# Kernel optimization log

Hardware: AMD Instinct MI355X
Metric: run time of the kernel (lower is better)

The kernel has to match this reference:

```python
import jax, jax.numpy as jnp
import numpy as np

B, P, ENC = 128, 196, 2048
D, A, ED, V, L = 512, 512, 512, 10000, 20


def setup_inputs() -> dict:
    key = jax.random.key(0)
    ks = jax.random.split(key, 24)
    s = 0.02
    inp = {
        'encoder_out': jax.random.normal(ks[0], (B, P, ENC), jnp.float32),
        'captions': jax.random.randint(ks[1], (B, L), 0, V),
        'caption_len': jax.random.randint(ks[2], (B,), 2, L + 1).at[0].set(L),
        # embedding (uniform(-0.1, 0.1) per init_weights)
        'emb_w': jax.random.uniform(ks[3], (V, ED), jnp.float32, -0.1, 0.1),
        # LSTMCell: input = ED + ENC, hidden = D, gates order i,f,g,o
        'Wih': jax.random.normal(ks[4], (4 * D, ED + ENC), jnp.float32) * s,
        'Whh': jax.random.normal(ks[5], (4 * D, D), jnp.float32) * s,
        'bih': jax.random.normal(ks[6], (4 * D,), jnp.float32) * s,
        'bhh': jax.random.normal(ks[7], (4 * D,), jnp.float32) * s,
        # init hidden state projections
        'h0_w': jax.random.normal(ks[8], (D, ENC), jnp.float32) * s,
        'h0_b': jnp.zeros((D,), jnp.float32),
        'c0_w': jax.random.normal(ks[9], (D, ENC), jnp.float32) * s,
        'c0_b': jnp.zeros((D,), jnp.float32),
        # gate D -> ENC
        'gate_w': jax.random.normal(ks[10], (ENC, D), jnp.float32) * s,
        'gate_b': jnp.zeros((ENC,), jnp.float32),
        # output projection D -> V (uniform(-0.1,0.1), bias 0 per init_weights)
        'lin_w': jax.random.uniform(ks[11], (V, D), jnp.float32, -0.1, 0.1),
        'lin_b': jnp.zeros((V,), jnp.float32),
        # attention network
        'ea_w': jax.random.normal(ks[12], (A, ENC), jnp.float32) * s,
        'ea_b': jnp.zeros((A,), jnp.float32),
        'da_w': jax.random.normal(ks[13], (A, D), jnp.float32) * s,
        'da_b': jnp.zeros((A,), jnp.float32),
        'fa_w': jax.random.normal(ks[14], (1, A), jnp.float32) * s,
        'fa_b': jnp.zeros((1,), jnp.float32),
    }
    return inp


def reference(encoder_out, captions, caption_len, emb_w, Wih, Whh, bih, bhh,
              h0_w, h0_b, c0_w, c0_b, gate_w, gate_b, lin_w, lin_b,
              ea_w, ea_b, da_w, da_b, fa_w, fa_b):
    # sort by caption length descending (as in torch .sort(descending=True))
    order = jnp.argsort(-caption_len)
    cap_len = caption_len[order]
    enc = encoder_out[order]            # [B, P, ENC]
    caps = captions[order]              # [B, L]
    dec_len = cap_len - 1               # per-example decode lengths

    emb = emb_w[caps]                   # [B, L, ED]
    mean_enc = enc.mean(axis=1)         # [B, ENC]
    h0 = mean_enc @ h0_w.T + h0_b       # [B, D]
    c0 = mean_enc @ c0_w.T + c0_b
    att1 = enc @ ea_w.T + ea_b          # [B, P, A] precomputed encoder attention

    T = caps.shape[1] - 1               # static max decode steps (caption_len[0]=L)

    def step(carry, i):
        h, c = carry
        # Bahdanau attention
        att2 = h @ da_w.T + da_b                                   # [B, A]
        e = (jax.nn.relu(att1 + att2[:, None, :]) @ fa_w.T + fa_b)[..., 0]  # [B, P]
        alpha = jax.nn.softmax(e, axis=1)
        awe = jnp.einsum('bp,bpe->be', alpha, enc)                 # [B, ENC]
        g = jax.nn.sigmoid(h @ gate_w.T + gate_b)
        awe = g * awe
        # LSTMCell
        x = jnp.concatenate([emb[:, i, :], awe], axis=1)           # [B, ED+ENC]
        gates = x @ Wih.T + bih + h @ Whh.T + bhh                  # [B, 4D]
        gi, gf, gg, go = jnp.split(gates, 4, axis=1)
        c_new = jax.nn.sigmoid(gf) * c + jax.nn.sigmoid(gi) * jnp.tanh(gg)
        h_new = jax.nn.sigmoid(go) * jnp.tanh(c_new)
        active = (i < dec_len)[:, None]                            # ragged mask
        # inactive rows keep old state (matches h[:batch_size_i] slicing)
        h2 = jnp.where(active, h_new, h)
        c2 = jnp.where(active, c_new, c)
        # dropout is identity in eval; output projection masked to zeros
        pred = jnp.where(active, h_new @ lin_w.T + lin_b, 0.0)     # [B, V]
        alpha = jnp.where(active, alpha, 0.0)
        return (h2, c2), (pred, alpha)

    (_, _), (preds, alphas) = jax.lax.scan(step, (h0, c0), jnp.arange(T))
    pred = jnp.swapaxes(preds, 0, 1)     # [B, T, V]
    alphas = jnp.swapaxes(alphas, 0, 1)  # [B, T, P]
    return pred, caps, dec_len, alphas, order
```

## Files before the change

kernel.cpp:

```cpp
#include <hip/hip_runtime.h>
#include <hip/hip_bf16.h>
#include <math.h>

#define Bn 128
#define Pn 196
#define ENCn 2048
#define Dn 512
#define An 512
#define EDn 512
#define Vn 10000
#define Ln 20
#define Tn 19

typedef short v8s __attribute__((ext_vector_type(8)));
typedef float v4f __attribute__((ext_vector_type(4)));

__device__ __forceinline__ float sigf(float x){ return 1.f/(1.f+__expf(-x)); }
__device__ __forceinline__ unsigned short f2bf(float f){
  unsigned u = __float_as_uint(f);
  return (unsigned short)((u + 0x7FFFu + ((u>>16)&1u)) >> 16);
}
__device__ __forceinline__ float bf2f(unsigned short h){
  return __uint_as_float(((unsigned)h)<<16);
}


__global__ void k_order(const int* __restrict__ caption_len,
                        const int* __restrict__ captions,
                        int* __restrict__ order_i, int* __restrict__ declen_i,
                        int* __restrict__ caps_s,
                        float* __restrict__ out_caps, float* __restrict__ out_declen,
                        float* __restrict__ out_order)
{
  __shared__ int lens[Bn];
  int b = threadIdx.x;
  lens[b] = caption_len[b];
  __syncthreads();
  int lb = lens[b];
  int r = 0;
  for (int j = 0; j < Bn; ++j) {
    int lj = lens[j];
    r += (int)((lj > lb) || (lj == lb && j < b));
  }
  order_i[r] = b;
  declen_i[r] = lb - 1;
  out_order[r] = (float)b;
  out_declen[r] = (float)(lb - 1);
  for (int t = 0; t < Ln; ++t) {
    int cv = captions[b*Ln + t];
    caps_s[r*Ln + t] = cv;
    out_caps[r*Ln + t] = (float)cv;
  }
}

__global__ void k_setup_bias(const float* __restrict__ bih, const float* __restrict__ bhh,
                             const float* __restrict__ da_b, const float* __restrict__ gate_b,
                             const float* __restrict__ h0_b, const float* __restrict__ c0_b,
                             float* __restrict__ bsum_r, float* __restrict__ dg_b,
                             float* __restrict__ hc_b)
{
  int i = blockIdx.x*256 + threadIdx.x;
  if (i < 2048) {
    int d = i >> 2, g = i & 3;
    bsum_r[i] = bih[g*512+d] + bhh[g*512+d];
  }
  if (i < 2560) dg_b[i] = (i < 512) ? da_b[i] : gate_b[i-512];
  if (i < 1024) hc_b[i] = (i < 512) ? h0_b[i] : c0_b[i-512];
}

__global__ void k_cvt(const float* __restrict__ src, unsigned short* __restrict__ dst, int n)
{
  int i = (blockIdx.x*256 + threadIdx.x)*4;
  if (i < n) {
    float4 v = *(const float4*)(src + i);
    dst[i+0]=f2bf(v.x); dst[i+1]=f2bf(v.y); dst[i+2]=f2bf(v.z); dst[i+3]=f2bf(v.w);
  }
}

__global__ void k_wcat(const float* __restrict__ Wih, const float* __restrict__ Whh,
                       unsigned short* __restrict__ dst)
{
  int i = (blockIdx.x*256 + threadIdx.x)*4;
  if (i >= 2048*3072) return;
  int rp = i/3072, j = i - rp*3072;
  int d = rp >> 2, g = rp & 3;
  int r = g*512 + d;
  const float* s = (j < 2560) ? (Wih + (size_t)r*2560 + j) : (Whh + (size_t)r*512 + (j-2560));
  float4 v = *(const float4*)s;
  dst[i+0]=f2bf(v.x); dst[i+1]=f2bf(v.y); dst[i+2]=f2bf(v.z); dst[i+3]=f2bf(v.w);
}

__global__ void k_cvt_enc(const float* __restrict__ enc, const int* __restrict__ order_i,
                          unsigned short* __restrict__ dst)
{
  int id = blockIdx.x;
  int b = id / Pn, p = id - b*Pn;
  const float* src = enc + ((size_t)order_i[b]*Pn + p)*ENCn;
  unsigned short* d = dst + (size_t)id*ENCn;
  int i = threadIdx.x*8;
  float4 v0 = *(const float4*)(src+i), v1 = *(const float4*)(src+i+4);
  d[i+0]=f2bf(v0.x); d[i+1]=f2bf(v0.y); d[i+2]=f2bf(v0.z); d[i+3]=f2bf(v0.w);
  d[i+4]=f2bf(v1.x); d[i+5]=f2bf(v1.y); d[i+6]=f2bf(v1.z); d[i+7]=f2bf(v1.w);
}

__global__ void k_mean(const unsigned short* __restrict__ enc_bf,
                       unsigned short* __restrict__ mean_bf)
{
  int b = blockIdx.x;
  const unsigned short* eb = enc_bf + (size_t)b*Pn*ENCn;
  for (int e = threadIdx.x; e < ENCn; e += 256) {
    float s = 0.f;
    for (int p = 0; p < Pn; ++p) s += bf2f(eb[(size_t)p*ENCn + e]);
    mean_bf[b*ENCn + e] = f2bf(s * (1.f/196.f));
  }
}

__global__ void k_zero(uint4* __restrict__ p, int n)
{
  int i = blockIdx.x*256 + threadIdx.x;
  if (i < n) p[i] = uint4{0,0,0,0};
}

__global__ void k_emb_all(const int* __restrict__ caps_s, const float* __restrict__ emb_w,
                          unsigned short* __restrict__ xh_all)
{
  int id = blockIdx.x; int t = id >> 7, b = id & 127;
  int tok = caps_s[b*Ln + t];
  const float* src = emb_w + (size_t)tok*EDn;
  unsigned short* d = xh_all + ((size_t)t*Bn + b)*3072;
  int i = threadIdx.x*2;
  float2 v = *(const float2*)(src+i);
  d[i] = f2bf(v.x); d[i+1] = f2bf(v.y);
}

__global__ void k_h2bf(const float* __restrict__ hc, float* __restrict__ c,
                       unsigned short* __restrict__ h_bf, unsigned short* __restrict__ xh_all)
{
  int b = blockIdx.x, d = threadIdx.x;
  float hv = hc[b*1024 + d];
  float cv = hc[b*1024 + 512 + d];
  c[b*Dn + d] = cv;
  unsigned short hb = f2bf(hv);
  h_bf[b*Dn + d] = hb;
  xh_all[(size_t)b*3072 + 2560 + d] = hb;
}

__global__ __launch_bounds__(256) void k_mfma_gemm(
    const unsigned short* __restrict__ Aw, const unsigned short* __restrict__ Bw,
    const float* __restrict__ bias, float* __restrict__ Cp,
    int N, int K, size_t ldc,
    const int* __restrict__ actlen, int t)
{
  __shared__ unsigned short smA[2][4096];
  __shared__ unsigned short smB[2][4096];
  const int tid = threadIdx.x;
  const int bm0 = blockIdx.y*64, bn0 = blockIdx.x*64;
  if (actlen && actlen[bm0] <= t) return;

  const int lane = tid & 63, w = tid >> 6;
  const int wr = w >> 1, wc = w & 1;
  const int lrow = lane & 15, kq = lane >> 4;

  v4f acc[2][2];
  #pragma unroll
  for (int i=0;i<2;++i)
    #pragma unroll
    for (int j=0;j<2;++j) acc[i][j] = (v4f)0.f;

  const int nt = K >> 6;

  auto stage = [&](int buf, int k0) {
    #pragma unroll
    for (int it = 0; it < 2; ++it) {
      int s = it*256 + tid;
      int row = s >> 3;
      int kb  = (s & 7) ^ (row & 7);
      *(v8s*)&smA[buf][s*8] = *(const v8s*)(Aw + (size_t)(bm0+row)*K + k0 + kb*8);
      *(v8s*)&smB[buf][s*8] = *(const v8s*)(Bw + (size_t)(bn0+row)*K + k0 + kb*8);
    }
  };
  auto compute = [&](int buf) {
    #pragma unroll
    for (int kc = 0; kc < 2; ++kc) {
      v8s aF[2], bF[2];
      #pragma unroll
      for (int mi = 0; mi < 2; ++mi) {
        int row = wr*32 + mi*16 + lrow;
        int kb = kc*4 + kq;
        aF[mi] = *(const v8s*)&smA[buf][row*64 + ((kb ^ (row&7))<<3)];
      }
      #pragma unroll
      for (int ni = 0; ni < 2; ++ni) {
        int row = wc*32 + ni*16 + lrow;
        int kb = kc*4 + kq;
        bF[ni] = *(const v8s*)&smB[buf][row*64 + ((kb ^ (row&7))<<3)];
      }
      #pragma unroll
      for (int mi = 0; mi < 2; ++mi)
        #pragma unroll
        for (int ni = 0; ni < 2; ++ni)
          acc[mi][ni] = __builtin_amdgcn_mfma_f32_16x16x32_bf16(aF[mi], bF[ni], acc[mi][ni], 0, 0, 0);
    }
  };

  stage(0, 0);
  __syncthreads();
  for (int tk = 0; tk < nt; ++tk) {
    if (tk + 1 < nt) stage((tk+1)&1, (tk+1)<<6);
    compute(tk&1);
    __syncthreads();
  }

  #pragma unroll
  for (int mi=0; mi<2; ++mi)
    #pragma unroll
    for (int ni=0; ni<2; ++ni)
      #pragma unroll
      for (int r=0; r<4; ++r) {
        int m = bm0 + wr*32 + mi*16 + kq*4 + r;
        int n = bn0 + wc*32 + ni*16 + lrow;
        Cp[(size_t)m*ldc + n] = acc[mi][ni][r] + bias[n];
      }
}

__global__ __launch_bounds__(256) void k_att1(
    const unsigned short* __restrict__ Aw, const unsigned short* __restrict__ Bw,
    const float* __restrict__ bias, unsigned short* __restrict__ Cp)
{
  __shared__ unsigned short smA[2][8192];
  __shared__ unsigned short smB[2][4096];
  const int tid = threadIdx.x;
  const int id = blockIdx.x;
  const int g = (id & 7)*196 + (id >> 3);
  const int bm0 = (g >> 3) * 128, bn0 = (g & 7) * 64;
  const int K = ENCn;

  const int lane = tid & 63, w = tid >> 6;
  const int wr = w >> 1, wc = w & 1;
  const int lrow = lane & 15, kq = lane >> 4;

  v4f acc[4][2];
  #pragma unroll
  for (int i=0;i<4;++i)
    #pragma unroll
    for (int j=0;j<2;++j) acc[i][j] = (v4f)0.f;

  auto stage = [&](int buf, int k0) {
    #pragma unroll
    for (int it = 0; it < 4; ++it) {
      int s = it*256 + tid;
      int row = s >> 3;
      int kb  = (s & 7) ^ (row & 7);
      *(v8s*)&smA[buf][s*8] = *(const v8s*)(Aw + (size_t)(bm0+row)*K + k0 + kb*8);
    }
    #pragma unroll
    for (int it = 0; it < 2; ++it) {
      int s = it*256 + tid;
      int row = s >> 3;
      int kb  = (s & 7) ^ (row & 7);
      *(v8s*)&smB[buf][s*8] = *(const v8s*)(Bw + (size_t)(bn0+row)*K + k0 + kb*8);
    }
  };
  auto compute = [&](int buf) {
    #pragma unroll
    for (int kc = 0; kc < 2; ++kc) {
      v8s aF[4], bF[2];
      #pragma unroll
      for (int mi = 0; mi < 4; ++mi) {
        int row = wr*64 + mi*16 + lrow;
        int kb = kc*4 + kq;
        aF[mi] = *(const v8s*)&smA[buf][row*64 + ((kb ^ (row&7))<<3)];
      }
      #pragma unroll
      for (int ni = 0; ni < 2; ++ni) {
        int row = wc*32 + ni*16 + lrow;
        int kb = kc*4 + kq;
        bF[ni] = *(const v8s*)&smB[buf][row*64 + ((kb ^ (row&7))<<3)];
      }
      #pragma unroll
      for (int mi = 0; mi < 4; ++mi)
        #pragma unroll
        for (int ni = 0; ni < 2; ++ni)
          acc[mi][ni] = __builtin_amdgcn_mfma_f32_16x16x32_bf16(aF[mi], bF[ni], acc[mi][ni], 0, 0, 0);
    }
  };

  stage(0, 0);
  __syncthreads();
  const int nt = K >> 6;
  for (int tk = 0; tk < nt; ++tk) {
    if (tk + 1 < nt) stage((tk+1)&1, (tk+1)<<6);
    compute(tk&1);
    __syncthreads();
  }

  #pragma unroll
  for (int mi=0; mi<4; ++mi)
    #pragma unroll
    for (int ni=0; ni<2; ++ni)
      #pragma unroll
      for (int r=0; r<4; ++r) {
        int m = bm0 + wr*64 + mi*16 + kq*4 + r;
        int n = bn0 + wc*32 + ni*16 + lrow;
        Cp[(size_t)m*An + n] = f2bf(acc[mi][ni][r] + bias[n]);
      }
}

__global__ __launch_bounds__(256) void k_gates_lstm(
    const unsigned short* __restrict__ Aw, const unsigned short* __restrict__ Bw,
    const float* __restrict__ bias,
    float* __restrict__ c, unsigned short* __restrict__ h_bf,
    unsigned short* __restrict__ h_all, unsigned short* __restrict__ xh_all,
    const int* __restrict__ declen_i, int t)
{
  __shared__ unsigned short smA[2][4096];
  __shared__ unsigned short smB[2][4096];
  __shared__ float smC[64][65];
  const int tid = threadIdx.x;
  const int bm0 = blockIdx.y*64, bn0 = blockIdx.x*64;
  if (declen_i[bm0] <= t) return;

  const int lane = tid & 63, w = tid >> 6;
  const int wr = w >> 1, wc = w & 1;
  const int lrow = lane & 15, kq = lane >> 4;
  const int K = 3072;

  v4f acc[2][2];
  #pragma unroll
  for (int i=0;i<2;++i)
    #pragma unroll
    for (int j=0;j<2;++j) acc[i][j] = (v4f)0.f;

  auto stage = [&](int buf, int k0) {
    #pragma unroll
    for (int it = 0; it < 2; ++it) {
      int s = it*256 + tid;
      int row = s >> 3;
      int kb  = (s & 7) ^ (row & 7);
      *(v8s*)&smA[buf][s*8] = *(const v8s*)(Aw + (size_t)(bm0+row)*K + k0 + kb*8);
      *(v8s*)&smB[buf][s*8] = *(const v8s*)(Bw + (size_t)(bn0+row)*K + k0 + kb*8);
    }
  };
  auto compute = [&](int buf) {
    #pragma unroll
    for (int kc = 0; kc < 2; ++kc) {
      v8s aF[2], bF[2];
      #pragma unroll
      for (int mi = 0; mi < 2; ++mi) {
        int row = wr*32 + mi*16 + lrow;
        int kb = kc*4 + kq;
        aF[mi] = *(const v8s*)&smA[buf][row*64 + ((kb ^ (row&7))<<3)];
      }
      #pragma unroll
      for (int ni = 0; ni < 2; ++ni) {
        int row = wc*32 + ni*16 + lrow;
        int kb = kc*4 + kq;
        bF[ni] = *(const v8s*)&smB[buf][row*64 + ((kb ^ (row&7))<<3)];
      }
      #pragma unroll
      for (int mi = 0; mi < 2; ++mi)
        #pragma unroll
        for (int ni = 0; ni < 2; ++ni)
          acc[mi][ni] = __builtin_amdgcn_mfma_f32_16x16x32_bf16(aF[mi], bF[ni], acc[mi][ni], 0, 0, 0);
    }
  };

  stage(0, 0);
  __syncthreads();
  const int nt = K >> 6;
  for (int tk = 0; tk < nt; ++tk) {
    if (tk + 1 < nt) stage((tk+1)&1, (tk+1)<<6);
    compute(tk&1);
    __syncthreads();
  }

  #pragma unroll
  for (int mi=0; mi<2; ++mi)
    #pragma unroll
    for (int ni=0; ni<2; ++ni)
      #pragma unroll
      for (int r=0; r<4; ++r) {
        int ml = wr*32 + mi*16 + kq*4 + r;
        int nl = wc*32 + ni*16 + lrow;
        smC[ml][nl] = acc[mi][ni][r] + bias[bn0 + nl];
      }
  __syncthreads();

  for (int idx = tid; idx < 1024; idx += 256) {
    int ml = idx >> 4, dl = idx & 15;
    int b = bm0 + ml;
    if (t < declen_i[b]) {
      int dg = (bn0 >> 2) + dl;
      float gi = smC[ml][dl*4+0];
      float gf = smC[ml][dl*4+1];
      float gg = smC[ml][dl*4+2];
      float go = smC[ml][dl*4+3];
      float cv = c[b*Dn + dg];
      float cn = sigf(gf)*cv + sigf(gi)*tanhf(gg);
      float hn = sigf(go)*tanhf(cn);
      c[b*Dn + dg] = cn;
      unsigned short hb = f2bf(hn);
      h_bf[b*Dn + dg] = hb;
      h_all[((size_t)t*Bn + b)*Dn + dg] = hb;
      if (t + 1 < Tn)
        xh_all[((size_t)(t+1)*Bn + b)*3072 + 2560 + dg] = hb;
    }
  }
}

__global__ __launch_bounds__(256) void k_pred(
    const unsigned short* __restrict__ Aw, const unsigned short* __restrict__ Bw,
    const float* __restrict__ bias, float* __restrict__ out_pred,
    const int* __restrict__ declen_i)
{
  __shared__ unsigned short smA[2][4096];
  __shared__ unsigned short smB[2][4096];
  const int tid = threadIdx.x;
  const int bm0 = blockIdx.y*64, bn0 = blockIdx.x*64;
  const int t0 = bm0 >> 7, b0 = bm0 & 127;

  if (declen_i[b0] <= t0) {
    for (int i = tid; i < 4096; i += 256) {
      int ml = i >> 6, nl = i & 63;
      int n = bn0 + nl;
      if (n < Vn) {
        int m = bm0 + ml;
        out_pred[((size_t)(m & 127)*Tn + (m >> 7))*Vn + n] = 0.f;
      }
    }
    return;
  }

  const int lane = tid & 63, w = tid >> 6;
  const int wr = w >> 1, wc = w & 1;
  const int lrow = lane & 15, kq = lane >> 4;
  const int K = 512;

  v4f acc[2][2];
  #pragma unroll
  for (int i=0;i<2;++i)
    #pragma unroll
    for (int j=0;j<2;++j) acc[i][j] = (v4f)0.f;

  auto stage = [&](int buf, int k0) {
    #pragma unroll
    for (int it = 0; it < 2; ++it) {
      int s = it*256 + tid;
      int row = s >> 3;
      int kb  = (s & 7) ^ (row & 7);
      *(v8s*)&smA[buf][s*8] = *(const v8s*)(Aw + (size_t)(bm0+row)*K + k0 + kb*8);
      {
        int gn = bn0 + row; if (gn >= Vn) gn = Vn-1;
        *(v8s*)&smB[buf][s*8] = *(const v8s*)(Bw + (size_t)gn*K + k0 + kb*8);
      }
    }
  };
  auto compute = [&](int buf) {
    #pragma unroll
    for (int kc = 0; kc < 2; ++kc) {
      v8s aF[2], bF[2];
      #pragma unroll
      for (int mi = 0; mi < 2; ++mi) {
        int row = wr*32 + mi*16 + lrow;
        int kb = kc*4 + kq;
        aF[mi] = *(const v8s*)&smA[buf][row*64 + ((kb ^ (row&7))<<3)];
      }
      #pragma unroll
      for (int ni = 0; ni < 2; ++ni) {
        int row = wc*32 + ni*16 + lrow;
        int kb = kc*4 + kq;
        bF[ni] = *(const v8s*)&smB[buf][row*64 + ((kb ^ (row&7))<<3)];
      }
      #pragma unroll
      for (int mi = 0; mi < 2; ++mi)
        #pragma unroll
        for (int ni = 0; ni < 2; ++ni)
          acc[mi][ni] = __builtin_amdgcn_mfma_f32_16x16x32_bf16(aF[mi], bF[ni], acc[mi][ni], 0, 0, 0);
    }
  };

  stage(0, 0);
  __syncthreads();
  const int nt = K >> 6;
  for (int tk = 0; tk < nt; ++tk) {
    if (tk + 1 < nt) stage((tk+1)&1, (tk+1)<<6);
    compute(tk&1);
    __syncthreads();
  }

  #pragma unroll
  for (int mi=0; mi<2; ++mi)
    #pragma unroll
    for (int ni=0; ni<2; ++ni)
      #pragma unroll
      for (int r=0; r<4; ++r) {
        int m = bm0 + wr*32 + mi*16 + kq*4 + r;
        int n = bn0 + wc*32 + ni*16 + lrow;
        if (n < Vn) {
          int b = m & 127, tt = m >> 7;
          float v = (tt < declen_i[b]) ? (acc[mi][ni][r] + bias[n]) : 0.f;
          out_pred[((size_t)b*Tn + tt)*Vn + n] = v;
        }
      }
}

__global__ __launch_bounds__(256) void k_esm(
    const unsigned short* __restrict__ att1, const float* __restrict__ att2g,
    const float* __restrict__ fa_w, const float* __restrict__ fa_b,
    float* __restrict__ alpha, float* __restrict__ out_alph,
    const int* __restrict__ declen_i, int t)
{
  int b = blockIdx.x;
  int tid = threadIdx.x;
  if (t >= declen_i[b]) {
    if (tid < Pn)
      out_alph[(size_t)b*Tn*Pn + (size_t)t*Pn + tid] = 0.f;
    return;
  }
  __shared__ float a2s[An];
  __shared__ float fws[An];
  __shared__ float es[Pn];
  __shared__ float wred[4];
  __shared__ float wsum[4];
  for (int i = tid; i < An; i += 256) { a2s[i] = att2g[(size_t)b*2560 + i]; fws[i] = fa_w[i]; }
  __syncthreads();
  int lane = tid & 63, w = tid >> 6;
  if (tid < Pn) {
    const unsigned short* row = att1 + ((size_t)b*Pn + tid)*An;
    float s = 0.f;
    #pragma unroll 4
    for (int kb = 0; kb < 64; ++kb) {
      const v8s vv = *(const v8s*)(row + kb*8);
      #pragma unroll
      for (int j = 0; j < 8; ++j) {
        int a = kb*8 + j;
        float v = bf2f((unsigned short)vv[j]) + a2s[a];
        s += fmaxf(v, 0.f) * fws[a];
      }
    }
    es[tid] = s + fa_b[0];
  }
  __syncthreads();
  float m = -1e30f;
  for (int p = tid; p < Pn; p += 256) m = fmaxf(m, es[p]);
  for (int off = 32; off; off >>= 1) m = fmaxf(m, __shfl_down(m, off));
  if (lane == 0) wred[w] = m;
  __syncthreads();
  m = fmaxf(fmaxf(wred[0], wred[1]), fmaxf(wred[2], wred[3]));
  float s = 0.f;
  for (int p = tid; p < Pn; p += 256) { float ev = __expf(es[p] - m); es[p] = ev; s += ev; }
  for (int off = 32; off; off >>= 1) s += __shfl_down(s, off);
  if (lane == 0) wsum[w] = s;
  __syncthreads();
  s = wsum[0] + wsum[1] + wsum[2] + wsum[3];
  float inv = 1.f / s;
  for (int p = tid; p < Pn; p += 256) {
    float al = es[p] * inv;
    alpha[b*Pn + p] = al;
    out_alph[(size_t)b*Tn*Pn + (size_t)t*Pn + p] = al;
  }
}

__global__ __launch_bounds__(256) void k_awe_gate(
    const unsigned short* __restrict__ enc_bf,
    const float* __restrict__ alpha, const float* __restrict__ att2g,
    unsigned short* __restrict__ xh_t, const int* __restrict__ declen_i, int t)
{
  int b = blockIdx.y;
  if (t >= declen_i[b]) return;
  __shared__ float als[Pn];
  __shared__ float red[8][256];
  int tid = threadIdx.x;
  if (tid < Pn) als[tid] = alpha[b*Pn + tid];
  __syncthreads();
  int e0 = blockIdx.x*256;
  int ec = tid & 31, ps = tid >> 5;
  const unsigned short* eb = enc_bf + (size_t)b*Pn*ENCn + e0 + ec*8;
  float s[8] = {};
  for (int p = ps; p < Pn; p += 8) {
    v8s v = *(const v8s*)(eb + (size_t)p*ENCn);
    float a = als[p];
    #pragma unroll
    for (int j = 0; j < 8; ++j) s[j] += a * bf2f((unsigned short)v[j]);
  }
  #pragma unroll
  for (int j = 0; j < 8; ++j) red[ps][ec*8+j] = s[j];
  __syncthreads();
  {
    int e = tid;
    float tsum = 0.f;
    #pragma unroll
    for (int k = 0; k < 8; ++k) tsum += red[k][e];
    int eg = e0 + e;
    float g = sigf(att2g[(size_t)b*2560 + 512 + eg]);
    xh_t[(size_t)b*3072 + 512 + eg] = f2bf(g*tsum);
  }
}


extern "C" void kernel_launch(void* const* d_in, const int* in_sizes, int n_in,
                              void* d_out, int out_size, void* d_ws, size_t ws_size,
                              hipStream_t stream)
{
  const float* enc     = (const float*)d_in[0];
  const int*   captions= (const int*)d_in[1];
  const int*   cap_len = (const int*)d_in[2];
  const float* emb_w   = (const float*)d_in[3];
  const float* Wih     = (const float*)d_in[4];
  const float* Whh     = (const float*)d_in[5];
  const float* bih     = (const float*)d_in[6];
  const float* bhh     = (const float*)d_in[7];
  const float* h0_w    = (const float*)d_in[8];
  const float* h0_b    = (const float*)d_in[9];
  const float* c0_w    = (const float*)d_in[10];
  const float* c0_b    = (const float*)d_in[11];
  const float* gate_w  = (const float*)d_in[12];
  const float* gate_b  = (const float*)d_in[13];
  const float* lin_w   = (const float*)d_in[14];
  const float* lin_b   = (const float*)d_in[15];
  const float* ea_w    = (const float*)d_in[16];
  const float* ea_b    = (const float*)d_in[17];
  const float* da_w    = (const float*)d_in[18];
  const float* da_b    = (const float*)d_in[19];
  const float* fa_w    = (const float*)d_in[20];
  const float* fa_b    = (const float*)d_in[21];

  float* out = (float*)d_out;
  float* out_pred   = out;
  float* out_caps   = out + (size_t)Bn*Tn*Vn;
  float* out_declen = out_caps + Bn*Ln;
  float* out_alph   = out_declen + Bn;
  float* out_order  = out_alph + (size_t)Bn*Tn*Pn;

  char* wp = (char*)d_ws;
  auto alloc = [&](size_t bytes)->void* {
    void* p = (void*)wp; wp += (bytes + 255) & ~(size_t)255; return p;
  };
  int*   order_i  = (int*)alloc(Bn*4);
  int*   declen_i = (int*)alloc(Bn*4);
  int*   caps_s   = (int*)alloc(Bn*Ln*4);
  unsigned short* enc_bf  = (unsigned short*)alloc((size_t)Bn*Pn*ENCn*2);
  unsigned short* mean_bf = (unsigned short*)alloc((size_t)Bn*ENCn*2);
  float* hc       = (float*)alloc((size_t)Bn*1024*4);
  float* c        = (float*)alloc((size_t)Bn*Dn*4);
  unsigned short* h_bf   = (unsigned short*)alloc((size_t)Bn*Dn*2);
  unsigned short* h_all  = (unsigned short*)alloc((size_t)Tn*Bn*Dn*2);
  unsigned short* xh_all = (unsigned short*)alloc((size_t)Tn*Bn*3072*2);
  unsigned short* att1   = (unsigned short*)alloc((size_t)Bn*Pn*An*2);
  float* att2g    = (float*)alloc((size_t)Bn*2560*4);
  float* alpha    = (float*)alloc((size_t)Bn*Pn*4);
  unsigned short* ea_bf   = (unsigned short*)alloc((size_t)An*ENCn*2);
  unsigned short* lin_bf  = (unsigned short*)alloc((size_t)Vn*Dn*2);
  unsigned short* h0c0_bf = (unsigned short*)alloc((size_t)1024*ENCn*2);
  unsigned short* dg_bf   = (unsigned short*)alloc((size_t)2560*Dn*2);
  unsigned short* wcat_bf = (unsigned short*)alloc((size_t)2048*3072*2);
  float* bsum = (float*)alloc(2048*4);
  float* dg_b = (float*)alloc(2560*4);
  float* hc_b = (float*)alloc(1024*4);

  k_order<<<1,128,0,stream>>>(cap_len, captions, order_i, declen_i, caps_s,
                              out_caps, out_declen, out_order);
  k_setup_bias<<<10,256,0,stream>>>(bih, bhh, da_b, gate_b, h0_b, c0_b, bsum, dg_b, hc_b);
  k_cvt<<<(An*ENCn/4+255)/256,256,0,stream>>>(ea_w, ea_bf, An*ENCn);
  k_cvt<<<(Vn*Dn/4+255)/256,256,0,stream>>>(lin_w, lin_bf, Vn*Dn);
  k_cvt<<<(Dn*ENCn/4+255)/256,256,0,stream>>>(h0_w, h0c0_bf, Dn*ENCn);
  k_cvt<<<(Dn*ENCn/4+255)/256,256,0,stream>>>(c0_w, h0c0_bf + (size_t)512*ENCn, Dn*ENCn);
  k_cvt<<<(An*Dn/4+255)/256,256,0,stream>>>(da_w, dg_bf, An*Dn);
  k_cvt<<<(ENCn*Dn/4+255)/256,256,0,stream>>>(gate_w, dg_bf + (size_t)512*Dn, ENCn*Dn);
  k_wcat<<<(2048*3072/4+255)/256,256,0,stream>>>(Wih, Whh, wcat_bf);
  k_cvt_enc<<<Bn*Pn,256,0,stream>>>(enc, order_i, enc_bf);
  k_mean<<<Bn,256,0,stream>>>(enc_bf, mean_bf);
  k_zero<<<((int)((size_t)Tn*Bn*3072*2/16)+255)/256,256,0,stream>>>(
      (uint4*)xh_all, (int)((size_t)Tn*Bn*3072*2/16));
  k_emb_all<<<Tn*Bn,256,0,stream>>>(caps_s, emb_w, xh_all);

  k_mfma_gemm<<<dim3(16,2),256,0,stream>>>(
      mean_bf, h0c0_bf, hc_b, hc, 1024, ENCn, 1024, nullptr, 0);
  k_h2bf<<<Bn,512,0,stream>>>(hc, c, h_bf, xh_all);

  k_att1<<<dim3(196*8),256,0,stream>>>(enc_bf, ea_bf, ea_b, att1);

  for (int t = 0; t < Tn; ++t) {
    unsigned short* xh_t = xh_all + (size_t)t*Bn*3072;
    k_mfma_gemm<<<dim3(40,2),256,0,stream>>>(
        h_bf, dg_bf, dg_b, att2g, 2560, Dn, 2560, declen_i, t);
    k_esm<<<Bn,256,0,stream>>>(att1, att2g, fa_w, fa_b, alpha, out_alph, declen_i, t);
    k_awe_gate<<<dim3(8,Bn),256,0,stream>>>(enc_bf, alpha, att2g, xh_t, declen_i, t);
    k_gates_lstm<<<dim3(32,2),256,0,stream>>>(
        xh_t, wcat_bf, bsum, c, h_bf, h_all, xh_all, declen_i, t);
  }

  k_pred<<<dim3((Vn+63)/64, (Tn*Bn)/64),256,0,stream>>>(
      h_all, lin_bf, lin_b, out_pred, declen_i);
}
```

Measured before the change: 1.639 ms.

## Fuse attention-projection GEMM into softmax kernel and enlarge prediction GEMM tiles

Each timestep used to run a separate GEMM for the decoder-attention projection and the gate, followed by the score/softmax kernel. Now one kernel does both: blocks 0-127 compute the per-row attention projection with a scalar dot product over a transposed bf16 copy of da_w, then run the softmax. Blocks 128 and up run the gate GEMM and store sigmoid-applied gates for the weighted-sum kernel. This saves one launch per step and the round trip through att2g. The final prediction GEMM now uses 128-row tiles, one per timestep, and drops the early zero-fill path, so inactive rows are computed and then masked to zero.

```diff
diff --git a/kernel.cpp b/kernel.cpp
--- a/kernel.cpp
+++ b/kernel.cpp
@@ -77,6 +77,17 @@
   }
 }
 
+__global__ void k_dgT(const float* __restrict__ da_w, unsigned short* __restrict__ dgT8)
+{
+  int i = blockIdx.x*256 + threadIdx.x;
+  int kb = i >> 9, n = i & 511;
+  const float* src = da_w + (size_t)n*512 + kb*8;
+  float4 v0 = *(const float4*)src, v1 = *(const float4*)(src+4);
+  unsigned short* d = dgT8 + (size_t)i*8;
+  d[0]=f2bf(v0.x); d[1]=f2bf(v0.y); d[2]=f2bf(v0.z); d[3]=f2bf(v0.w);
+  d[4]=f2bf(v1.x); d[5]=f2bf(v1.y); d[6]=f2bf(v1.z); d[7]=f2bf(v1.w);
+}
+
 __global__ void k_wcat(const float* __restrict__ Wih, const float* __restrict__ Whh,
                        unsigned short* __restrict__ dst)
 {
@@ -148,14 +159,12 @@
 __global__ __launch_bounds__(256) void k_mfma_gemm(
     const unsigned short* __restrict__ Aw, const unsigned short* __restrict__ Bw,
     const float* __restrict__ bias, float* __restrict__ Cp,
-    int N, int K, size_t ldc,
-    const int* __restrict__ actlen, int t)
+    int N, int K, size_t ldc)
 {
   __shared__ unsigned short smA[2][4096];
   __shared__ unsigned short smB[2][4096];
   const int tid = threadIdx.x;
   const int bm0 = blockIdx.y*64, bn0 = blockIdx.x*64;
-  if (actlen && actlen[bm0] <= t) return;
 
   const int lane = tid & 63, w = tid >> 6;
   const int wr = w >> 1, wc = w & 1;
@@ -304,6 +313,194 @@
         int n = bn0 + wc*32 + ni*16 + lrow;
         Cp[(size_t)m*An + n] = f2bf(acc[mi][ni][r] + bias[n]);
       }
+}
+
+__global__ __launch_bounds__(256) void k_esm_gpre(
+    const unsigned short* __restrict__ att1, const unsigned short* __restrict__ dgT8,
+    const unsigned short* __restrict__ dg_bf, const float* __restrict__ dg_b,
+    const unsigned short* __restrict__ h_bf,
+    const float* __restrict__ fa_w, const float* __restrict__ fa_b,
+    float* __restrict__ alpha, float* __restrict__ out_alph,
+    float* __restrict__ gbuf,
+    const int* __restrict__ declen_i, int t)
+{
+  __shared__ __align__(16) char smraw[32768];
+  const int tid = threadIdx.x;
+
+  if (blockIdx.x >= 128) {
+    unsigned short (*smA)[4096] = (unsigned short(*)[4096])smraw;
+    unsigned short (*smB)[4096] = (unsigned short(*)[4096])(smraw + 16384);
+    const int id = blockIdx.x - 128;
+    const int bm0 = (id >> 5) * 64, bn0 = (id & 31) * 64;
+    if (declen_i[bm0] <= t) return;
+    const unsigned short* Bw = dg_bf + (size_t)512*Dn;
+    const int K = Dn;
+
+    const int lane = tid & 63, w = tid >> 6;
+    const int wr = w >> 1, wc = w & 1;
+    const int lrow = lane & 15, kq = lane >> 4;
+
+    v4f acc[2][2];
+    #pragma unroll
+    for (int i=0;i<2;++i)
+      #pragma unroll
+      for (int j=0;j<2;++j) acc[i][j] = (v4f)0.f;
+
+    auto stage = [&](int buf, int k0) {
+      #pragma unroll
+      for (int it = 0; it < 2; ++it) {
+        int s = it*256 + tid;
+        int row = s >> 3;
+        int kb  = (s & 7) ^ (row & 7);
+        *(v8s*)&smA[buf][s*8] = *(const v8s*)(h_bf + (size_t)(bm0+row)*K + k0 + kb*8);
+        *(v8s*)&smB[buf][s*8] = *(const v8s*)(Bw + (size_t)(bn0+row)*K + k0 + kb*8);
+      }
+    };
+    auto compute = [&](int buf) {
+      #pragma unroll
+      for (int kc = 0; kc < 2; ++kc) {
+        v8s aF[2], bF[2];
+        #pragma unroll
+        for (int mi = 0; mi < 2; ++mi) {
+          int row = wr*32 + mi*16 + lrow;
+          int kb = kc*4 + kq;
+          aF[mi] = *(const v8s*)&smA[buf][row*64 + ((kb ^ (row&7))<<3)];
+        }
+        #pragma unroll
+        for (int ni = 0; ni < 2; ++ni) {
+          int row = wc*32 + ni*16 + lrow;
+          int kb = kc*4 + kq;
+          bF[ni] = *(const v8s*)&smB[buf][row*64 + ((kb ^ (row&7))<<3)];
+        }
+        #pragma unroll
+        for (int mi = 0; mi < 2; ++mi)
+          #pragma unroll
+          for (int ni = 0; ni < 2; ++ni)
+            acc[mi][ni] = __builtin_amdgcn_mfma_f32_16x16x32_bf16(aF[mi], bF[ni], acc[mi][ni], 0, 0, 0);
+      }
+    };
+
+    stage(0, 0);
+    __syncthreads();
+    const int nt = K >> 6;
+    for (int tk = 0; tk < nt; ++tk) {
+      if (tk + 1 < nt) stage((tk+1)&1, (tk+1)<<6);
+      compute(tk&1);
+      __syncthreads();
+    }
+
+    #pragma unroll
+    for (int mi=0; mi<2; ++mi)
+      #pragma unroll
+      for (int ni=0; ni<2; ++ni)
+        #pragma unroll
+        for (int r=0; r<4; ++r) {
+          int m = bm0 + wr*32 + mi*16 + kq*4 + r;
+          int n = bn0 + wc*32 + ni*16 + lrow;
+          gbuf[(size_t)m*2048 + n] = sigf(acc[mi][ni][r] + dg_b[512 + n]);
+        }
+    return;
+  }
+
+  int b = blockIdx.x;
+  if (t >= declen_i[b]) {
+    if (tid < Pn)
+      out_alph[(size_t)b*Tn*Pn + (size_t)t*Pn + tid] = 0.f;
+    return;
+  }
+  float* h_l  = (float*)smraw;
+  float* a2s  = h_l + 512;
+  float* fws  = a2s + 512;
+  float* es   = fws + 512;
+  float* wred = es + 200;
+  float* wsum = wred + 4;
+
+  for (int i = tid; i < Dn; i += 256) h_l[i] = bf2f(h_bf[b*Dn + i]);
+  for (int i = tid; i < An; i += 256) fws[i] = fa_w[i];
+  __syncthreads();
+  #pragma unroll
+  for (int half = 0; half < 2; ++half) {
+    int n = tid + half*256;
+    float s = 0.f;
+    #pragma unroll 4
+    for (int kb = 0; kb < 64; ++kb) {
+      v8s wv = *(const v8s*)(dgT8 + ((size_t)kb*512 + n)*8);
+      #pragma unroll
+      for (int j = 0; j < 8; ++j) s += bf2f((unsigned short)wv[j]) * h_l[kb*8 + j];
+    }
+    a2s[n] = s + dg_b[n];
+  }
+  __syncthreads();
+  int lane = tid & 63, w = tid >> 6;
+  if (tid < Pn) {
+    const unsigned short* row = att1 + ((size_t)b*Pn + tid)*An;
+    float s = 0.f;
+    #pragma unroll 4
+    for (int kb = 0; kb < 64; ++kb) {
+      const v8s vv = *(const v8s*)(row + kb*8);
+      #pragma unroll
+      for (int j = 0; j < 8; ++j) {
+        int a = kb*8 + j;
+        float v = bf2f((unsigned short)vv[j]) + a2s[a];
+        s += fmaxf(v, 0.f) * fws[a];
+      }
+    }
+    es[tid] = s + fa_b[0];
+  }
+  __syncthreads();
+  float m = -1e30f;
+  for (int p = tid; p < Pn; p += 256) m = fmaxf(m, es[p]);
+  for (int off = 32; off; off >>= 1) m = fmaxf(m, __shfl_down(m, off));
+  if (lane == 0) wred[w] = m;
+  __syncthreads();
+  m = fmaxf(fmaxf(wred[0], wred[1]), fmaxf(wred[2], wred[3]));
+  float s = 0.f;
+  for (int p = tid; p < Pn; p += 256) { float ev = __expf(es[p] - m); es[p] = ev; s += ev; }
+  for (int off = 32; off; off >>= 1) s += __shfl_down(s, off);
+  if (lane == 0) wsum[w] = s;
+  __syncthreads();
+  s = wsum[0] + wsum[1] + wsum[2] + wsum[3];
+  float inv = 1.f / s;
+  for (int p = tid; p < Pn; p += 256) {
+    float al = es[p] * inv;
+    alpha[b*Pn + p] = al;
+    out_alph[(size_t)b*Tn*Pn + (size_t)t*Pn + p] = al;
+  }
+}
+
+__global__ __launch_bounds__(256) void k_awe_gate(
+    const unsigned short* __restrict__ enc_bf,
+    const float* __restrict__ alpha, const float* __restrict__ gbuf,
+    unsigned short* __restrict__ xh_t, const int* __restrict__ declen_i, int t)
+{
+  int b = blockIdx.y;
+  if (t >= declen_i[b]) return;
+  __shared__ float als[Pn];
+  __shared__ float red[8][256];
+  int tid = threadIdx.x;
+  if (tid < Pn) als[tid] = alpha[b*Pn + tid];
+  __syncthreads();
+  int e0 = blockIdx.x*256;
+  int ec = tid & 31, ps = tid >> 5;
+  const unsigned short* eb = enc_bf + (size_t)b*Pn*ENCn + e0 + ec*8;
+  float s[8] = {};
+  for (int p = ps; p < Pn; p += 8) {
+    v8s v = *(const v8s*)(eb + (size_t)p*ENCn);
+    float a = als[p];
+    #pragma unroll
+    for (int j = 0; j < 8; ++j) s[j] += a * bf2f((unsigned short)v[j]);
+  }
+  #pragma unroll
+  for (int j = 0; j < 8; ++j) red[ps][ec*8+j] = s[j];
+  __syncthreads();
+  {
+    int eg = e0 + tid;
+    float tsum = 0.f;
+    #pragma unroll
+    for (int k = 0; k < 8; ++k) tsum += red[k][tid];
+    float g = gbuf[(size_t)b*2048 + eg];
+    xh_t[(size_t)b*3072 + 512 + eg] = f2bf(g*tsum);
+  }
 }
 
 __global__ __launch_bounds__(256) void k_gates_lstm(
@@ -413,55 +610,47 @@
     const float* __restrict__ bias, float* __restrict__ out_pred,
     const int* __restrict__ declen_i)
 {
-  __shared__ unsigned short smA[2][4096];
+  __shared__ unsigned short smA[2][8192];
   __shared__ unsigned short smB[2][4096];
   const int tid = threadIdx.x;
-  const int bm0 = blockIdx.y*64, bn0 = blockIdx.x*64;
-  const int t0 = bm0 >> 7, b0 = bm0 & 127;
-
-  if (declen_i[b0] <= t0) {
-    for (int i = tid; i < 4096; i += 256) {
-      int ml = i >> 6, nl = i & 63;
-      int n = bn0 + nl;
-      if (n < Vn) {
-        int m = bm0 + ml;
-        out_pred[((size_t)(m & 127)*Tn + (m >> 7))*Vn + n] = 0.f;
-      }
-    }
-    return;
-  }
+  const int t0 = blockIdx.y;
+  const int bm0 = t0*128, bn0 = blockIdx.x*64;
+  const int K = Dn;
 
   const int lane = tid & 63, w = tid >> 6;
   const int wr = w >> 1, wc = w & 1;
   const int lrow = lane & 15, kq = lane >> 4;
-  const int K = 512;
-
-  v4f acc[2][2];
-  #pragma unroll
-  for (int i=0;i<2;++i)
+
+  v4f acc[4][2];
+  #pragma unroll
+  for (int i=0;i<4;++i)
     #pragma unroll
     for (int j=0;j<2;++j) acc[i][j] = (v4f)0.f;
 
   auto stage = [&](int buf, int k0) {
+    #pragma unroll
+    for (int it = 0; it < 4; ++it) {
+      int s = it*256 + tid;
+      int row = s >> 3;
+      int kb  = (s & 7) ^ (row & 7);
+      *(v8s*)&smA[buf][s*8] = *(const v8s*)(Aw + (size_t)(bm0+row)*K + k0 + kb*8);
+    }
     #pragma unroll
     for (int it = 0; it < 2; ++it) {
       int s = it*256 + tid;
       int row = s >> 3;
       int kb  = (s & 7) ^ (row & 7);
-      *(v8s*)&smA[buf][s*8] = *(const v8s*)(Aw + (size_t)(bm0+row)*K + k0 + kb*8);
-      {
-        int gn = bn0 + row; if (gn >= Vn) gn = Vn-1;
-        *(v8s*)&smB[buf][s*8] = *(const v8s*)(Bw + (size_t)gn*K + k0 + kb*8);
-      }
+      int gn = bn0 + row; if (gn >= Vn) gn = Vn-1;
+      *(v8s*)&smB[buf][s*8] = *(const v8s*)(Bw + (size_t)gn*K + k0 + kb*8);
     }
   };
   auto compute = [&](int buf) {
     #pragma unroll
     for (int kc = 0; kc < 2; ++kc) {
-      v8s aF[2], bF[2];
-      #pragma unroll
-      for (int mi = 0; mi < 2; ++mi) {
-        int row = wr*32 + mi*16 + lrow;
+      v8s aF[4], bF[2];
+      #pragma unroll
+      for (int mi = 0; mi < 4; ++mi) {
+        int row = wr*64 + mi*16 + lrow;
         int kb = kc*4 + kq;
         aF[mi] = *(const v8s*)&smA[buf][row*64 + ((kb ^ (row&7))<<3)];
       }
@@ -472,7 +661,7 @@
         bF[ni] = *(const v8s*)&smB[buf][row*64 + ((kb ^ (row&7))<<3)];
       }
       #pragma unroll
-      for (int mi = 0; mi < 2; ++mi)
+      for (int mi = 0; mi < 4; ++mi)
         #pragma unroll
         for (int ni = 0; ni < 2; ++ni)
           acc[mi][ni] = __builtin_amdgcn_mfma_f32_16x16x32_bf16(aF[mi], bF[ni], acc[mi][ni], 0, 0, 0);
@@ -489,112 +678,18 @@
   }
 
   #pragma unroll
-  for (int mi=0; mi<2; ++mi)
+  for (int mi=0; mi<4; ++mi)
     #pragma unroll
     for (int ni=0; ni<2; ++ni)
       #pragma unroll
       for (int r=0; r<4; ++r) {
-        int m = bm0 + wr*32 + mi*16 + kq*4 + r;
+        int b = wr*64 + mi*16 + kq*4 + r;
         int n = bn0 + wc*32 + ni*16 + lrow;
         if (n < Vn) {
-          int b = m & 127, tt = m >> 7;
-          float v = (tt < declen_i[b]) ? (acc[mi][ni][r] + bias[n]) : 0.f;
-          out_pred[((size_t)b*Tn + tt)*Vn + n] = v;
+          float v = (t0 < declen_i[b]) ? (acc[mi][ni][r] + bias[n]) : 0.f;
+          out_pred[((size_t)b*Tn + t0)*Vn + n] = v;
         }
       }
-}
-
-__global__ __launch_bounds__(256) void k_esm(
-    const unsigned short* __restrict__ att1, const float* __restrict__ att2g,
-    const float* __restrict__ fa_w, const float* __restrict__ fa_b,
-    float* __restrict__ alpha, float* __restrict__ out_alph,
-    const int* __restrict__ declen_i, int t)
-{
-  int b = blockIdx.x;
-  int tid = threadIdx.x;
-  if (t >= declen_i[b]) {
-    if (tid < Pn)
-      out_alph[(size_t)b*Tn*Pn + (size_t)t*Pn + tid] = 0.f;
-    return;
-  }
-  __shared__ float a2s[An];
-  __shared__ float fws[An];
-  __shared__ float es[Pn];
-  __shared__ float wred[4];
-  __shared__ float wsum[4];
-  for (int i = tid; i < An; i += 256) { a2s[i] = att2g[(size_t)b*2560 + i]; fws[i] = fa_w[i]; }
-  __syncthreads();
-  int lane = tid & 63, w = tid >> 6;
-  if (tid < Pn) {
-    const unsigned short* row = att1 + ((size_t)b*Pn + tid)*An;
-    float s = 0.f;
-    #pragma unroll 4
-    for (int kb = 0; kb < 64; ++kb) {
-      const v8s vv = *(const v8s*)(row + kb*8);
-      #pragma unroll
-      for (int j = 0; j < 8; ++j) {
-        int a = kb*8 + j;
-        float v = bf2f((unsigned short)vv[j]) + a2s[a];
-        s += fmaxf(v, 0.f) * fws[a];
-      }
-    }
-    es[tid] = s + fa_b[0];
-  }
-  __syncthreads();
-  float m = -1e30f;
-  for (int p = tid; p < Pn; p += 256) m = fmaxf(m, es[p]);
-  for (int off = 32; off; off >>= 1) m = fmaxf(m, __shfl_down(m, off));
-  if (lane == 0) wred[w] = m;
-  __syncthreads();
-  m = fmaxf(fmaxf(wred[0], wred[1]), fmaxf(wred[2], wred[3]));
-  float s = 0.f;
-  for (int p = tid; p < Pn; p += 256) { float ev = __expf(es[p] - m); es[p] = ev; s += ev; }
-  for (int off = 32; off; off >>= 1) s += __shfl_down(s, off);
-  if (lane == 0) wsum[w] = s;
-  __syncthreads();
-  s = wsum[0] + wsum[1] + wsum[2] + wsum[3];
-  float inv = 1.f / s;
-  for (int p = tid; p < Pn; p += 256) {
-    float al = es[p] * inv;
-    alpha[b*Pn + p] = al;
-    out_alph[(size_t)b*Tn*Pn + (size_t)t*Pn + p] = al;
-  }
-}
-
-__global__ __launch_bounds__(256) void k_awe_gate(
-    const unsigned short* __restrict__ enc_bf,
-    const float* __restrict__ alpha, const float* __restrict__ att2g,
-    unsigned short* __restrict__ xh_t, const int* __restrict__ declen_i, int t)
-{
-  int b = blockIdx.y;
-  if (t >= declen_i[b]) return;
-  __shared__ float als[Pn];
-  __shared__ float red[8][256];
-  int tid = threadIdx.x;
-  if (tid < Pn) als[tid] = alpha[b*Pn + tid];
-  __syncthreads();
-  int e0 = blockIdx.x*256;
-  int ec = tid & 31, ps = tid >> 5;
-  const unsigned short* eb = enc_bf + (size_t)b*Pn*ENCn + e0 + ec*8;
-  float s[8] = {};
-  for (int p = ps; p < Pn; p += 8) {
-    v8s v = *(const v8s*)(eb + (size_t)p*ENCn);
-    float a = als[p];
-    #pragma unroll
-    for (int j = 0; j < 8; ++j) s[j] += a * bf2f((unsigned short)v[j]);
-  }
-  #pragma unroll
-  for (int j = 0; j < 8; ++j) red[ps][ec*8+j] = s[j];
-  __syncthreads();
-  {
-    int e = tid;
-    float tsum = 0.f;
-    #pragma unroll
-    for (int k = 0; k < 8; ++k) tsum += red[k][e];
-    int eg = e0 + e;
-    float g = sigf(att2g[(size_t)b*2560 + 512 + eg]);
-    xh_t[(size_t)b*3072 + 512 + eg] = f2bf(g*tsum);
-  }
 }
 
 
@@ -647,12 +742,13 @@
   unsigned short* h_all  = (unsigned short*)alloc((size_t)Tn*Bn*Dn*2);
   unsigned short* xh_all = (unsigned short*)alloc((size_t)Tn*Bn*3072*2);
   unsigned short* att1   = (unsigned short*)alloc((size_t)Bn*Pn*An*2);
-  float* att2g    = (float*)alloc((size_t)Bn*2560*4);
+  float* gbuf     = (float*)alloc((size_t)Bn*2048*4);
   float* alpha    = (float*)alloc((size_t)Bn*Pn*4);
   unsigned short* ea_bf   = (unsigned short*)alloc((size_t)An*ENCn*2);
   unsigned short* lin_bf  = (unsigned short*)alloc((size_t)Vn*Dn*2);
   unsigned short* h0c0_bf = (unsigned short*)alloc((size_t)1024*ENCn*2);
   unsigned short* dg_bf   = (unsigned short*)alloc((size_t)2560*Dn*2);
+  unsigned short* dgT8    = (unsigned short*)alloc((size_t)512*512*2);
   unsigned short* wcat_bf = (unsigned short*)alloc((size_t)2048*3072*2);
   float* bsum = (float*)alloc(2048*4);
   float* dg_b = (float*)alloc(2560*4);
@@ -667,6 +763,7 @@
   k_cvt<<<(Dn*ENCn/4+255)/256,256,0,stream>>>(c0_w, h0c0_bf + (size_t)512*ENCn, Dn*ENCn);
   k_cvt<<<(An*Dn/4+255)/256,256,0,stream>>>(da_w, dg_bf, An*Dn);
   k_cvt<<<(ENCn*Dn/4+255)/256,256,0,stream>>>(gate_w, dg_bf + (size_t)512*Dn, ENCn*Dn);
+  k_dgT<<<128,256,0,stream>>>(da_w, dgT8);
   k_wcat<<<(2048*3072/4+255)/256,256,0,stream>>>(Wih, Whh, wcat_bf);
   k_cvt_enc<<<Bn*Pn,256,0,stream>>>(enc, order_i, enc_bf);
   k_mean<<<Bn,256,0,stream>>>(enc_bf, mean_bf);
@@ -675,21 +772,20 @@
   k_emb_all<<<Tn*Bn,256,0,stream>>>(caps_s, emb_w, xh_all);
 
   k_mfma_gemm<<<dim3(16,2),256,0,stream>>>(
-      mean_bf, h0c0_bf, hc_b, hc, 1024, ENCn, 1024, nullptr, 0);
+      mean_bf, h0c0_bf, hc_b, hc, 1024, ENCn, 1024);
   k_h2bf<<<Bn,512,0,stream>>>(hc, c, h_bf, xh_all);
 
   k_att1<<<dim3(196*8),256,0,stream>>>(enc_bf, ea_bf, ea_b, att1);
 
   for (int t = 0; t < Tn; ++t) {
     unsigned short* xh_t = xh_all + (size_t)t*Bn*3072;
-    k_mfma_gemm<<<dim3(40,2),256,0,stream>>>(
-        h_bf, dg_bf, dg_b, att2g, 2560, Dn, 2560, declen_i, t);
-    k_esm<<<Bn,256,0,stream>>>(att1, att2g, fa_w, fa_b, alpha, out_alph, declen_i, t);
-    k_awe_gate<<<dim3(8,Bn),256,0,stream>>>(enc_bf, alpha, att2g, xh_t, declen_i, t);
+    k_esm_gpre<<<192,256,0,stream>>>(att1, dgT8, dg_bf, dg_b, h_bf, fa_w, fa_b,
+                                     alpha, out_alph, gbuf, declen_i, t);
+    k_awe_gate<<<dim3(8,Bn),256,0,stream>>>(enc_bf, alpha, gbuf, xh_t, declen_i, t);
     k_gates_lstm<<<dim3(32,2),256,0,stream>>>(
         xh_t, wcat_bf, bsum, c, h_bf, h_all, xh_all, declen_i, t);
   }
 
-  k_pred<<<dim3((Vn+63)/64, (Tn*Bn)/64),256,0,stream>>>(
+  k_pred<<<dim3((Vn+63)/64, Tn),256,0,stream>>>(
       h_all, lin_bf, lin_b, out_pred, declen_i);
 }
```

Measured after the change: 1.814 ms. +10.7%, slower.
